# Kernel tuning notes

Hardware: AMD Instinct MI355X
Metric: run time of the kernel (lower is better)

Reference implementation:

```python
import jax, jax.numpy as jnp
import numpy as np
from jax import lax

IMG = 1024
STRIDES = (4, 8, 16, 32, 64)
SIZE_BASES = (32, 64, 128, 256, 512)
SCALES = (8.0,)
RATIOS = (0.5, 1.0, 2.0)
PRE_NMS = 2000
POST_NMS = 1000
NMS_THRESH = 0.7
B = 4


def _level_anchors(stride, size_base):
    """Anchors [G*G*A, 4] in xyxy, centered on grid cells."""
    g = IMG // stride
    cs = (jnp.arange(g, dtype=jnp.float32) + 0.5) * stride
    cy, cx = jnp.meshgrid(cs, cs, indexing='ij')          # [g,g]
    ctr = jnp.stack([cx.ravel(), cy.ravel()], axis=-1)    # [g*g, 2]
    wh = []
    for r in RATIOS:
        for s in SCALES:
            wh.append((size_base * s * np.sqrt(1.0 / r), size_base * s * np.sqrt(r)))
    wh = jnp.asarray(wh, jnp.float32)                     # [A, 2]
    x1y1 = ctr[:, None, :] - 0.5 * wh[None, :, :]
    x2y2 = ctr[:, None, :] + 0.5 * wh[None, :, :]
    return jnp.concatenate([x1y1, x2y2], axis=-1).reshape(-1, 4)


def _decode(anchors, deltas):
    wa = anchors[:, 2] - anchors[:, 0]
    ha = anchors[:, 3] - anchors[:, 1]
    cxa = anchors[:, 0] + 0.5 * wa
    cya = anchors[:, 1] + 0.5 * ha
    dx, dy, dw, dh = deltas[:, 0], deltas[:, 1], deltas[:, 2], deltas[:, 3]
    cx = dx * wa + cxa
    cy = dy * ha + cya
    w = jnp.exp(dw) * wa
    h = jnp.exp(dh) * ha
    return jnp.stack([cx - 0.5 * w, cy - 0.5 * h, cx + 0.5 * w, cy + 0.5 * h], axis=-1)


def _clip(boxes, info):
    h, w = info[0], info[1]
    x = jnp.clip(boxes[:, 0::2], 0.0, w - 1.0)
    y = jnp.clip(boxes[:, 1::2], 0.0, h - 1.0)
    return jnp.stack([x[:, 0], y[:, 0], x[:, 1], y[:, 1]], axis=-1)


def _iou_matrix(boxes):
    area = jnp.maximum(boxes[:, 2] - boxes[:, 0], 0.0) * jnp.maximum(boxes[:, 3] - boxes[:, 1], 0.0)
    lt = jnp.maximum(boxes[:, None, :2], boxes[None, :, :2])
    rb = jnp.minimum(boxes[:, None, 2:], boxes[None, :, 2:])
    wh = jnp.maximum(rb - lt, 0.0)
    inter = wh[..., 0] * wh[..., 1]
    return inter / jnp.maximum(area[:, None] + area[None, :] - inter, 1e-9)


def _nms_keep(boxes, thresh):
    """Boxes sorted by score desc. Returns boolean keep mask."""
    iou = _iou_matrix(boxes)
    n = boxes.shape[0]
    idx = jnp.arange(n)
    def body(i, keep):
        sup = keep[i] & (iou[i] > thresh) & (idx > i)
        return keep & ~sup
    return lax.fori_loop(0, n, body, jnp.ones((n,), bool))


def reference(probs0, probs1, probs2, probs3, probs4,
              reg0, reg1, reg2, reg3, reg4, img_info):
    anchors = [_level_anchors(s, b) for s, b in zip(STRIDES, SIZE_BASES)]
    probs = (probs0, probs1, probs2, probs3, probs4)
    regs = (reg0, reg1, reg2, reg3, reg4)

    def per_image(pr, rg, info):
        boxes_all, scores_all = [], []
        for a, p, r in zip(anchors, pr, rg):
            scores = p[:, 0]
            proposals = _clip(_decode(a, r), info)
            k = min(PRE_NMS, scores.shape[0])
            s, order = lax.top_k(scores, k)        # pre-NMS top-k, sorted desc
            bx = proposals[order]
            keep = _nms_keep(bx, NMS_THRESH)
            s = jnp.where(keep, s, -1.0)           # suppressed -> sentinel
            kp = min(POST_NMS, k)
            s2, o2 = lax.top_k(s, kp)              # post-NMS top-k per level
            boxes_all.append(bx[o2])
            scores_all.append(s2)
        ab = jnp.concatenate(boxes_all, axis=0)
        asc = jnp.concatenate(scores_all, axis=0)
        fs, fo = lax.top_k(asc, POST_NMS)          # merge levels, final top-k
        fb = jnp.where((fs >= 0.0)[:, None], ab[fo], 0.0)  # zero-pad invalid
        return fb

    fb = jax.vmap(per_image)(probs, regs, img_info)        # [B, POST, 4]
    bidx = jnp.broadcast_to(jnp.arange(B, dtype=fb.dtype)[:, None, None], (B, POST_NMS, 1))
    return jnp.concatenate([bidx, fb], axis=-1)            # [B, POST, 5]


def setup_inputs():
    key = jax.random.key(0)
    ks = jax.random.split(key, 10)
    grids = [IMG // s for s in STRIDES]
    A = [g * g * len(RATIOS) * len(SCALES) for g in grids]
    inp = {}
    for l in range(5):
        inp[f'probs{l}'] = jax.random.uniform(ks[l], (B, A[l], 2), dtype=jnp.float32)
        inp[f'reg{l}'] = 0.1 * jax.random.normal(ks[5 + l], (B, A[l], 4), dtype=jnp.float32)
    inp['img_info'] = jnp.tile(jnp.array([IMG, IMG, 1.0], jnp.float32), (B, 1))
    return inp
```

## Files before the change

### kernel.cpp

```cpp
#include <hip/hip_runtime.h>
#include <stdint.h>
#include <math.h>

#pragma clang fp contract(off)

#define NB 4
#define TOTA 261888
#define PRE 2000
#define POST 1000
#define CATN 4768
#define NBL 20
#define CANDCAP 4096
#define NBLK 4092
#define BPB 1023
#define HBLK 65

__device__ __forceinline__ unsigned keyF(float f) {
  unsigned u = __float_as_uint(f);
  return (u & 0x80000000u) ? ~u : (u | 0x80000000u);
}

__device__ __forceinline__ int lvlA(int l)   { switch (l) { case 0: return 196608; case 1: return 49152; case 2: return 12288; case 3: return 3072; default: return 768; } }
__device__ __forceinline__ int lvlOff(int l) { switch (l) { case 0: return 0; case 1: return 196608; case 2: return 245760; case 3: return 258048; default: return 261120; } }
__device__ __forceinline__ int lvlK(int l)   { return l == 4 ? 768 : 2000; }
__device__ __forceinline__ int lvlKP(int l)  { return l == 4 ? 768 : 1000; }
__device__ __forceinline__ int lvlBlkStart(int l) { switch (l) { case 0: return 0; case 1: return 768; case 2: return 960; case 3: return 1008; default: return 1020; } }
__device__ __forceinline__ int lvlBlkCnt(int l)   { switch (l) { case 0: return 768; case 1: return 192; case 2: return 48; case 3: return 12; default: return 3; } }

struct InPtrs {
  const float *p0, *p1, *p2, *p3, *p4;
  const float *r0, *r1, *r2, *r3, *r4;
  const float *info;
};

__device__ __forceinline__ void gaToLvl(int ga, int& l, int& off) {
  if (ga < 196608)      { l = 0; off = 0; }
  else if (ga < 245760) { l = 1; off = 196608; }
  else if (ga < 258048) { l = 2; off = 245760; }
  else if (ga < 261120) { l = 3; off = 258048; }
  else                  { l = 4; off = 261120; }
}

__device__ __forceinline__ void fatMap(int s, int& l, int& seg) {
  if (s < 48)      { l = 0; seg = s; }
  else if (s < 60) { l = 1; seg = s - 48; }
  else if (s < 63) { l = 2; seg = s - 60; }
  else if (s == 63){ l = 3; seg = 0; }
  else             { l = 4; seg = 0; }
}

__global__ __launch_bounds__(256) void k_decode(InPtrs P, float4* __restrict__ props,
                                                float* __restrict__ scores) {
  int gid = blockIdx.x * 256 + threadIdx.x;
  if (gid >= NB * TOTA) return;
  int b = gid / TOTA, ga = gid % TOTA;
  int Al, off, lg; float st; double S; const float *prp, *rgp;
  if (ga < 196608)      { Al = 196608; off = 0;      lg = 8; st = 4.0f;  S = 256.0;  prp = P.p0; rgp = P.r0; }
  else if (ga < 245760) { Al = 49152;  off = 196608; lg = 7; st = 8.0f;  S = 512.0;  prp = P.p1; rgp = P.r1; }
  else if (ga < 258048) { Al = 12288;  off = 245760; lg = 6; st = 16.0f; S = 1024.0; prp = P.p2; rgp = P.r2; }
  else if (ga < 261120) { Al = 3072;   off = 258048; lg = 5; st = 32.0f; S = 2048.0; prp = P.p3; rgp = P.r3; }
  else                  { Al = 768;    off = 261120; lg = 4; st = 64.0f; S = 4096.0; prp = P.p4; rgp = P.r4; }
  int i = ga - off;
  int cell = i / 3, rr = i - cell * 3;
  int col = cell & ((1 << lg) - 1), row = cell >> lg;
  float cx0 = ((float)col + 0.5f) * st;
  float cy0 = ((float)row + 0.5f) * st;
  const double SQ2 = 1.4142135623730951;
  const double SQH = 0.7071067811865476;
  double swd = (rr == 0) ? SQ2 : (rr == 1 ? 1.0 : SQH);
  double shd = (rr == 0) ? SQH : (rr == 1 ? 1.0 : SQ2);
  float wf = (float)(S * swd), hf = (float)(S * shd);
  float ax1 = cx0 - 0.5f * wf, ay1 = cy0 - 0.5f * hf;
  float ax2 = cx0 + 0.5f * wf, ay2 = cy0 + 0.5f * hf;
  size_t base = (size_t)b * Al + i;
  float sc = prp[base * 2];
  float4 d4 = ((const float4*)rgp)[base];
  float dx = d4.x, dy = d4.y, dw = d4.z, dh = d4.w;
  float wa = ax2 - ax1, ha = ay2 - ay1;
  float cxa = ax1 + 0.5f * wa, cya = ay1 + 0.5f * ha;
  float cx = dx * wa + cxa, cy = dy * ha + cya;
  float w = (float)exp((double)dw) * wa;
  float h = (float)exp((double)dh) * ha;
  float x1 = cx - 0.5f * w, y1 = cy - 0.5f * h;
  float x2 = cx + 0.5f * w, y2 = cy + 0.5f * h;
  float Hc = P.info[b * 3 + 0] - 1.0f, Wc = P.info[b * 3 + 1] - 1.0f;
  float4 o;
  o.x = fminf(fmaxf(x1, 0.0f), Wc);
  o.y = fminf(fmaxf(y1, 0.0f), Hc);
  o.z = fminf(fmaxf(x2, 0.0f), Wc);
  o.w = fminf(fmaxf(y2, 0.0f), Hc);
  props[gid] = o;
  scores[gid] = sc;
}

__global__ __launch_bounds__(256) void k_hist8(const float* __restrict__ scores,
                                               unsigned* __restrict__ hist8) {
  __shared__ unsigned h[256];
  int blk = blockIdx.x;
  int b = blk / HBLK, s = blk % HBLK;
  int l, seg; fatMap(s, l, seg);
  int n = lvlA(l), off = lvlOff(l);
  int start = seg * 4096;
  int cnt_s = min(4096, n - start);
  int tid = threadIdx.x;
  h[tid] = 0;
  __syncthreads();
  const float* sc = scores + (size_t)b * TOTA + off + start;
  for (int q = tid; q < cnt_s; q += 256)
    atomicAdd(&h[keyF(sc[q]) >> 24], 1u);
  __syncthreads();
  unsigned v = h[tid];
  if (v) atomicAdd(&hist8[(b * 5 + l) * 256 + tid], v);
}

__global__ __launch_bounds__(256) void k_thr8(const unsigned* __restrict__ hist8,
                                              unsigned* __restrict__ c1r1) {
  __shared__ unsigned h[256];
  int bl = blockIdx.x, tid = threadIdx.x;
  h[tid] = hist8[bl * 256 + tid];
  __syncthreads();
  if (tid == 0) {
    unsigned K = (unsigned)lvlK(bl % 5), cum = 0; int c;
    for (c = 255; c > 0; --c) { if (cum + h[c] >= K) break; cum += h[c]; }
    c1r1[bl * 2] = (unsigned)c;
    c1r1[bl * 2 + 1] = K - cum;
  }
}

__global__ __launch_bounds__(256) void k_hist6(const float* __restrict__ scores,
                                               const unsigned* __restrict__ c1r1,
                                               unsigned* __restrict__ hist6) {
  __shared__ unsigned h[64];
  int blk = blockIdx.x;
  int b = blk / HBLK, s = blk % HBLK;
  int l, seg; fatMap(s, l, seg);
  int n = lvlA(l), off = lvlOff(l);
  int start = seg * 4096;
  int cnt_s = min(4096, n - start);
  int tid = threadIdx.x;
  int bl = b * 5 + l;
  unsigned c1 = c1r1[bl * 2];
  if (tid < 64) h[tid] = 0;
  __syncthreads();
  const float* sc = scores + (size_t)b * TOTA + off + start;
  for (int q = tid; q < cnt_s; q += 256) {
    unsigned key = keyF(sc[q]);
    if ((key >> 24) == c1) atomicAdd(&h[(key >> 18) & 63u], 1u);
  }
  __syncthreads();
  if (tid < 64) {
    unsigned v = h[tid];
    if (v) atomicAdd(&hist6[bl * 64 + tid], v);
  }
}

__global__ __launch_bounds__(64) void k_thr6(const unsigned* __restrict__ hist6,
                                             const unsigned* __restrict__ c1r1,
                                             unsigned* __restrict__ T14) {
  __shared__ unsigned h[64];
  int bl = blockIdx.x, tid = threadIdx.x;
  h[tid] = hist6[bl * 64 + tid];
  __syncthreads();
  if (tid == 0) {
    unsigned r1 = c1r1[bl * 2 + 1], cum = 0; int c;
    for (c = 63; c > 0; --c) { if (cum + h[c] >= r1) break; cum += h[c]; }
    T14[bl] = (c1r1[bl * 2] << 6) | (unsigned)c;
  }
}

__global__ __launch_bounds__(256) void k_cnt(const float* __restrict__ scores,
                                             const unsigned* __restrict__ T14,
                                             unsigned* __restrict__ blockCnt) {
  __shared__ unsigned ws[4];
  int gid = blockIdx.x * 256 + threadIdx.x;
  int tid = threadIdx.x;
  int b = gid / TOTA, ga = gid % TOTA;
  int l, off; gaToLvl(ga, l, off);
  int bl = b * 5 + l;
  bool pred = (keyF(scores[gid]) >> 18) >= T14[bl];
  unsigned long long m = __ballot(pred);
  if ((tid & 63) == 0) ws[tid >> 6] = (unsigned)__popcll(m);
  __syncthreads();
  if (tid == 0) blockCnt[blockIdx.x] = ws[0] + ws[1] + ws[2] + ws[3];
}

__global__ __launch_bounds__(1024) void k_scanblk(const unsigned* __restrict__ blockCnt,
                                                  unsigned* __restrict__ blockBase,
                                                  unsigned* __restrict__ cnt) {
  __shared__ unsigned a[4096];
  __shared__ unsigned ch[1024];
  int tid = threadIdx.x;
  int q0 = tid * 4;
  unsigned a0 = (q0 + 0 < NBLK) ? blockCnt[q0 + 0] : 0u;
  unsigned a1 = (q0 + 1 < NBLK) ? blockCnt[q0 + 1] : 0u;
  unsigned a2 = (q0 + 2 < NBLK) ? blockCnt[q0 + 2] : 0u;
  unsigned a3 = (q0 + 3 < NBLK) ? blockCnt[q0 + 3] : 0u;
  unsigned p0 = a0, p1 = p0 + a1, p2 = p1 + a2, p3 = p2 + a3;
  ch[tid] = p3;
  __syncthreads();
  for (int d = 1; d < 1024; d <<= 1) {
    unsigned t = (tid >= d) ? ch[tid - d] : 0u;
    __syncthreads();
    ch[tid] += t;
    __syncthreads();
  }
  unsigned cbase = (tid > 0) ? ch[tid - 1] : 0u;
  a[q0 + 0] = cbase + p0;
  a[q0 + 1] = cbase + p1;
  a[q0 + 2] = cbase + p2;
  a[q0 + 3] = cbase + p3;
  __syncthreads();
  for (int k = 0; k < 4; ++k) {
    int g = q0 + k;
    if (g < NBLK) {
      int b = g / BPB, r = g % BPB;
      int l = (r < 768) ? 0 : (r < 960) ? 1 : (r < 1008) ? 2 : (r < 1020) ? 3 : 4;
      int ss = b * BPB + lvlBlkStart(l);
      unsigned Eg = (g > 0) ? a[g - 1] : 0u;
      unsigned Es = (ss > 0) ? a[ss - 1] : 0u;
      blockBase[g] = Eg - Es;
    }
  }
  if (tid < NBL) {
    int b = tid / 5, l = tid % 5;
    int ss = b * BPB + lvlBlkStart(l);
    int ee = ss + lvlBlkCnt(l);
    unsigned Ee = a[ee - 1];
    unsigned Es = (ss > 0) ? a[ss - 1] : 0u;
    cnt[tid] = Ee - Es;
  }
}

__global__ __launch_bounds__(256) void k_fill(const float* __restrict__ scores,
                                              const unsigned* __restrict__ T14,
                                              const unsigned* __restrict__ blockBase,
                                              unsigned long long* __restrict__ cand) {
  __shared__ unsigned ws[4];
  int gid = blockIdx.x * 256 + threadIdx.x;
  int tid = threadIdx.x;
  int b = gid / TOTA, ga = gid % TOTA;
  int l, off; gaToLvl(ga, l, off);
  int bl = b * 5 + l;
  unsigned key = keyF(scores[gid]);
  bool pred = (key >> 18) >= T14[bl];
  unsigned long long m = __ballot(pred);
  int wv = tid >> 6, ln = tid & 63;
  if (ln == 0) ws[wv] = (unsigned)__popcll(m);
  __syncthreads();
  unsigned wo = 0;
  for (int q = 0; q < wv; ++q) wo += ws[q];
  unsigned pre = (unsigned)__popcll(m & ((1ull << ln) - 1ull));
  if (pred) {
    unsigned p = blockBase[blockIdx.x] + wo + pre;
    if (p < CANDCAP)
      cand[(size_t)bl * CANDCAP + p] =
          ((unsigned long long)key << 32) | (unsigned long long)(0xFFFFFFFFu - (unsigned)(ga - off));
  }
}

__global__ __launch_bounds__(256) void k_sortc(unsigned long long* __restrict__ cand,
                                               const unsigned* __restrict__ cnt) {
  __shared__ unsigned long long arr[512];
  int blk = blockIdx.x;
  int bl = blk >> 3, ch = blk & 7;
  int base = ch * 512;
  int num = (int)min(cnt[bl], (unsigned)CANDCAP);
  int tid = threadIdx.x;
  unsigned long long* cp = cand + (size_t)bl * CANDCAP + base;
  for (int q = tid; q < 512; q += 256)
    arr[q] = (base + q < num) ? cp[q] : 0ull;
  __syncthreads();
  for (int kk = 2; kk <= 512; kk <<= 1)
    for (int jj = kk >> 1; jj > 0; jj >>= 1) {
      for (int idx = tid; idx < 512; idx += 256) {
        int p2 = idx ^ jj;
        if (p2 > idx) {
          unsigned long long x = arr[idx], y = arr[p2];
          bool up = (idx & kk) == 0;
          if (up ? (x < y) : (x > y)) { arr[idx] = y; arr[p2] = x; }
        }
      }
      __syncthreads();
    }
  for (int q = tid; q < 512; q += 256) cp[q] = arr[q];
}

__global__ __launch_bounds__(256) void k_rank(const unsigned long long* __restrict__ cand,
                                              const float4* __restrict__ props,
                                              const float* __restrict__ scores,
                                              float4* __restrict__ sBox,
                                              float* __restrict__ sArea,
                                              float* __restrict__ sScore) {
  int gid = blockIdx.x * 256 + threadIdx.x;
  int bl = gid >> 12, p = gid & 4095;
  int b = bl / 5, l = bl % 5;
  int K = lvlK(l), off = lvlOff(l);
  const unsigned long long* cp = cand + (size_t)bl * CANDCAP;
  unsigned long long me = cp[p];
  int ch = p >> 9;
  int rank = p & 511;
  for (int c2 = 0; c2 < 8; ++c2) {
    if (c2 == ch) continue;
    const unsigned long long* d = cp + c2 * 512;
    int lo = 0, hi = 512;
    while (lo < hi) {
      int mid = (lo + hi) >> 1;
      if (d[mid] > me) lo = mid + 1; else hi = mid;
    }
    rank += lo;
  }
  if (rank < K) {
    unsigned idx = 0xFFFFFFFFu - (unsigned)(me & 0xFFFFFFFFull);
    float4 bx = props[(size_t)b * TOTA + off + idx];
    float area = fmaxf(bx.z - bx.x, 0.0f) * fmaxf(bx.w - bx.y, 0.0f);
    sBox[bl * PRE + rank] = bx;
    sArea[bl * PRE + rank] = area;
    sScore[bl * PRE + rank] = scores[(size_t)b * TOTA + off + idx];
  }
}

__global__ __launch_bounds__(256) void k_mask(const float4* __restrict__ sBox,
                                              const float* __restrict__ sArea,
                                              unsigned long long* __restrict__ mask) {
  int bi = blockIdx.x;
  int bl = bi >> 8, rem = bi & 255, ic = rem >> 3, jc = rem & 7;
  int l = bl % 5, K = lvlK(l);
  int i0 = ic * 64, j0 = jc * 256;
  if (i0 >= K || j0 >= K) return;
  if (jc * 4 + 3 < ic) return;
  int tid = threadIdx.x;
  __shared__ float4 jb[256];
  __shared__ float ja[256];
  int jend = min(256, K - j0);
  if (tid < jend) { jb[tid] = sBox[bl * PRE + j0 + tid]; ja[tid] = sArea[bl * PRE + j0 + tid]; }
  int ln = tid & 63, wsub = tid >> 6;
  int i = i0 + ln;
  int jw = jc * 4 + wsub;
  bool iv = i < K;
  float4 bi4 = make_float4(0.0f, 0.0f, 0.0f, 0.0f);
  float ai = 0.0f;
  if (iv) { bi4 = sBox[bl * PRE + i]; ai = sArea[bl * PRE + i]; }
  __syncthreads();
  int jbase = wsub * 64;
  int lim = jend - jbase;
  if (lim > 64) lim = 64;
  unsigned long long wacc = 0ull;
#pragma unroll 4
  for (int t = 0; t < lim; ++t) {
    float4 b4 = jb[jbase + t];
    float aj = ja[jbase + t];
    int j = j0 + jbase + t;
    bool pred = false;
    if (j > i) {
      float ltx = fmaxf(bi4.x, b4.x), lty = fmaxf(bi4.y, b4.y);
      float rbx = fminf(bi4.z, b4.z), rby = fminf(bi4.w, b4.w);
      float wx = fmaxf(rbx - ltx, 0.0f), wy = fmaxf(rby - lty, 0.0f);
      float inter = wx * wy;
      float den = fmaxf(ai + aj - inter, 1e-9f);
      pred = (inter / den) > 0.7f;
    }
    wacc |= ((unsigned long long)(pred ? 1u : 0u)) << t;
  }
  if (iv && jw >= ic && lim > 0)
    mask[((size_t)bl * PRE + i) * 32 + jw] = wacc;
}

__global__ __launch_bounds__(1024) void k_nms(const unsigned long long* __restrict__ mask,
                                              const float4* __restrict__ sBox,
                                              const float* __restrict__ sScore,
                                              float* __restrict__ catScore,
                                              float4* __restrict__ catBox) {
  __shared__ unsigned long long diag[PRE];
  __shared__ unsigned long long remv[32];
  __shared__ int list[1000];
  __shared__ int sTotal;
  int bl = blockIdx.x, b = bl / 5, l = bl % 5;
  int K = lvlK(l), KP = lvlKP(l), co = l * 1000;
  int tid = threadIdx.x;
  const unsigned long long* mrow = mask + (size_t)bl * PRE * 32;
  int c = tid & 31, g = tid >> 5;
  int nw = (K + 63) >> 6;
  for (int r = tid; r < K; r += 1024) diag[r] = mrow[(size_t)r * 32 + (r >> 6)];
  if (tid < 32) remv[tid] = 0ull;
  __syncthreads();
  unsigned long long w0 = 0ull, w1 = 0ull, nw0 = 0ull, nw1 = 0ull;
  {
    bool act = (c > 0) && (c < nw);
    int row0 = g, row1 = g + 32;
    if (act && row0 < K) w0 = mrow[(size_t)row0 * 32 + c];
    if (act && row1 < K) w1 = mrow[(size_t)row1 * 32 + c];
  }
  for (int t = 0; t < nw; ++t) {
    nw0 = 0ull; nw1 = 0ull;
    if (t + 1 < nw) {
      bool actn = (c > t + 1) && (c < nw);
      int row0 = (t + 1) * 64 + g, row1 = row0 + 32;
      if (actn && row0 < K) nw0 = mrow[(size_t)row0 * 32 + c];
      if (actn && row1 < K) nw1 = mrow[(size_t)row1 * 32 + c];
    }
    if (tid < 64) {
      int dr = t * 64 + tid;
      unsigned long long d = (dr < K) ? diag[dr] : 0ull;
      unsigned long long local = remv[t];
      int lim = min(64, K - t * 64);
      unsigned long long validm = (lim >= 64) ? ~0ull : ((1ull << lim) - 1ull);
      unsigned long long todo = (~local) & validm;
      while (todo) {
        int i2 = __ffsll((long long)todo) - 1;
        unsigned lo2 = __builtin_amdgcn_readlane((unsigned)d, i2);
        unsigned hi2 = __builtin_amdgcn_readlane((unsigned)(d >> 32), i2);
        unsigned long long dd = ((unsigned long long)hi2 << 32) | (unsigned long long)lo2;
        local |= dd;
        todo &= ~dd;
        todo &= ~(1ull << i2);
      }
      if (tid == 0) remv[t] = local;
    }
    __syncthreads();
    {
      unsigned long long local = remv[t];
      bool act = (c > t) && (c < nw);
      if (act) {
        unsigned long long acc = 0ull;
        int row0 = t * 64 + g, row1 = row0 + 32;
        if (row0 < K && !((local >> g) & 1ull)) acc |= w0;
        if (row1 < K && !((local >> (g + 32)) & 1ull)) acc |= w1;
        if (acc) atomicOr(&remv[c], acc);
      }
    }
    __syncthreads();
    w0 = nw0; w1 = nw1;
  }
  if (tid < 64) {
    int lane = tid;
    bool lv = lane < 32;
    unsigned long long remw = lv ? remv[lane] : 0ull;
    unsigned long long valid = 0ull;
    if (lv) {
      int rem = K - lane * 64;
      valid = (rem >= 64) ? ~0ull : (rem <= 0 ? 0ull : ((1ull << rem) - 1ull));
    }
    unsigned long long keepw = (~remw) & valid;
    unsigned long long suppw = remw & valid;
    unsigned long long lmask = (1ull << lane) - 1ull;
    int base = 0;
    for (int w2 = 0; w2 < 32 && base < KP; ++w2) {
      unsigned long long word = __shfl(keepw, w2);
      int pre = __popcll(word & lmask);
      if (((word >> lane) & 1ull) && (base + pre) < KP) list[base + pre] = w2 * 64 + lane;
      base += __popcll(word);
    }
    int totalKept = base;
    if (totalKept < KP) {
      int b2 = totalKept;
      for (int w2 = 0; w2 < 32 && b2 < KP; ++w2) {
        unsigned long long word = __shfl(suppw, w2);
        int pre = __popcll(word & lmask);
        if (((word >> lane) & 1ull) && (b2 + pre) < KP) list[b2 + pre] = w2 * 64 + lane;
        b2 += __popcll(word);
      }
    }
    if (lane == 0) sTotal = totalKept;
  }
  __syncthreads();
  int totalKept = sTotal;
  for (int t = tid; t < KP; t += 1024) {
    int j = list[t];
    float s = (t < totalKept) ? sScore[bl * PRE + j] : -1.0f;
    catScore[b * CATN + co + t] = s;
    catBox[b * CATN + co + t] = sBox[bl * PRE + j];
  }
}

__global__ __launch_bounds__(256) void k_final(const float* __restrict__ catScore,
                                               const float4* __restrict__ catBox,
                                               float* __restrict__ out) {
  int gid = blockIdx.x * 256 + threadIdx.x;
  if (gid >= NB * CATN) return;
  int b = gid / CATN, p = gid % CATN;
  int c = p / 1000; if (c > 4) c = 4;
  const float* cs = catScore + (size_t)b * CATN;
  float s = cs[p];
  unsigned long long me = ((unsigned long long)keyF(s) << 32) |
                          (unsigned long long)(0xFFFFFFFFu - (unsigned)p);
  int rank = p - c * 1000;
  for (int c2 = 0; c2 < 5; ++c2) {
    if (c2 == c) continue;
    int base = c2 * 1000, len = (c2 == 4) ? 768 : 1000;
    int lo = 0, hi = len;
    while (lo < hi) {
      int mid = (lo + hi) >> 1;
      int q = base + mid;
      unsigned long long k2 = ((unsigned long long)keyF(cs[q]) << 32) |
                              (unsigned long long)(0xFFFFFFFFu - (unsigned)q);
      if (k2 > me) lo = mid + 1; else hi = mid;
    }
    rank += lo;
  }
  if (rank < POST) {
    float4 bx = make_float4(0.0f, 0.0f, 0.0f, 0.0f);
    if (s >= 0.0f) bx = catBox[(size_t)b * CATN + p];
    float* o = out + ((size_t)b * POST + rank) * 5;
    o[0] = (float)b; o[1] = bx.x; o[2] = bx.y; o[3] = bx.z; o[4] = bx.w;
  }
}

extern "C" void kernel_launch(void* const* d_in, const int* in_sizes, int n_in,
                              void* d_out, int out_size, void* d_ws, size_t ws_size,
                              hipStream_t stream) {
  const int prSz[5] = {1572864, 393216, 98304, 24576, 6144};
  const int rgSz[5] = {3145728, 786432, 196608, 49152, 12288};
  const float* pr[5] = {nullptr, nullptr, nullptr, nullptr, nullptr};
  const float* rg[5] = {nullptr, nullptr, nullptr, nullptr, nullptr};
  const float* info = nullptr;
  for (int i = 0; i < n_in; ++i) {
    int s = in_sizes[i];
    bool m = false;
    for (int l = 0; l < 5; ++l) {
      if (s == prSz[l]) { pr[l] = (const float*)d_in[i]; m = true; break; }
      if (s == rgSz[l]) { rg[l] = (const float*)d_in[i]; m = true; break; }
    }
    if (!m && s == 12) info = (const float*)d_in[i];
  }
  InPtrs P;
  P.p0 = pr[0]; P.p1 = pr[1]; P.p2 = pr[2]; P.p3 = pr[3]; P.p4 = pr[4];
  P.r0 = rg[0]; P.r1 = rg[1]; P.r2 = rg[2]; P.r3 = rg[3]; P.r4 = rg[4];
  P.info = info;

  char* w = (char*)d_ws;
  float4* props = (float4*)w;                         w += (size_t)NB * TOTA * 16;
  float4* sBox = (float4*)w;                          w += (size_t)NBL * PRE * 16;
  float4* catBox = (float4*)w;                        w += (size_t)NB * CATN * 16;
  unsigned long long* mask = (unsigned long long*)w;  w += (size_t)NBL * PRE * 32 * 8;
  unsigned long long* cand = (unsigned long long*)w;  w += (size_t)NBL * CANDCAP * 8;
  float* scores = (float*)w;                          w += (size_t)NB * TOTA * 4;
  float* sArea = (float*)w;                           w += (size_t)NBL * PRE * 4;
  float* sScore = (float*)w;                          w += (size_t)NBL * PRE * 4;
  float* catScore = (float*)w;                        w += (size_t)NB * CATN * 4;
  unsigned* hist8 = (unsigned*)w;                     w += (size_t)NBL * 256 * 4;
  unsigned* hist6 = (unsigned*)w;                     w += (size_t)NBL * 64 * 4;
  unsigned* c1r1 = (unsigned*)w;                      w += (size_t)NBL * 2 * 4;
  unsigned* T14 = (unsigned*)w;                       w += (size_t)NBL * 4;
  unsigned* blockCnt = (unsigned*)w;                  w += (size_t)NBLK * 4;
  unsigned* blockBase = (unsigned*)w;                 w += (size_t)NBLK * 4;
  unsigned* cnt = (unsigned*)w;                       w += (size_t)NBL * 4;
  (void)ws_size; (void)out_size;

  hipMemsetAsync(hist8, 0, (size_t)NBL * (256 + 64) * 4, stream);

  k_decode<<<(NB * TOTA + 255) / 256, 256, 0, stream>>>(P, props, scores);
  k_hist8<<<NB * HBLK, 256, 0, stream>>>(scores, hist8);
  k_thr8<<<NBL, 256, 0, stream>>>(hist8, c1r1);
  k_hist6<<<NB * HBLK, 256, 0, stream>>>(scores, c1r1, hist6);
  k_thr6<<<NBL, 64, 0, stream>>>(hist6, c1r1, T14);
  k_cnt<<<NBLK, 256, 0, stream>>>(scores, T14, blockCnt);
  k_scanblk<<<1, 1024, 0, stream>>>(blockCnt, blockBase, cnt);
  k_fill<<<NBLK, 256, 0, stream>>>(scores, T14, blockBase, cand);
  k_sortc<<<NBL * 8, 256, 0, stream>>>(cand, cnt);
  k_rank<<<NBL * CANDCAP / 256, 256, 0, stream>>>(cand, props, scores, sBox, sArea, sScore);
  k_mask<<<NBL * 256, 256, 0, stream>>>(sBox, sArea, mask);
  k_nms<<<NBL, 1024, 0, stream>>>(mask, sBox, sScore, catScore, catBox);
  k_final<<<(NB * CATN + 255) / 256, 256, 0, stream>>>(catScore, catBox, (float*)d_out);
}
```

Baseline: 197.9 us.

## Drop precomputed IoU mask; compute suppression on the fly inside NMS kernel

Removes the separate k_mask kernel and the global IoU bitmask. The NMS kernel now loads boxes and areas into shared memory and computes only the per-tile diagonal masks. For each 64-box tile it then resolves the kept boxes serially, and every thread tests its own two candidate boxes against each kept box. This removes one launch and the large mask writes and reads, and it only computes IoU for boxes that are actually kept. In exchange, the IoU work now runs serially inside 20 blocks instead of being spread across many blocks.

Result: slower. 451.3 us (+128.0%).

```diff
diff --git a/kernel.cpp b/kernel.cpp
--- a/kernel.cpp
+++ b/kernel.cpp
@@ -319,92 +319,81 @@
   }
 }
 
-__global__ __launch_bounds__(256) void k_mask(const float4* __restrict__ sBox,
-                                              const float* __restrict__ sArea,
-                                              unsigned long long* __restrict__ mask) {
-  int bi = blockIdx.x;
-  int bl = bi >> 8, rem = bi & 255, ic = rem >> 3, jc = rem & 7;
-  int l = bl % 5, K = lvlK(l);
-  int i0 = ic * 64, j0 = jc * 256;
-  if (i0 >= K || j0 >= K) return;
-  if (jc * 4 + 3 < ic) return;
-  int tid = threadIdx.x;
-  __shared__ float4 jb[256];
-  __shared__ float ja[256];
-  int jend = min(256, K - j0);
-  if (tid < jend) { jb[tid] = sBox[bl * PRE + j0 + tid]; ja[tid] = sArea[bl * PRE + j0 + tid]; }
-  int ln = tid & 63, wsub = tid >> 6;
-  int i = i0 + ln;
-  int jw = jc * 4 + wsub;
-  bool iv = i < K;
-  float4 bi4 = make_float4(0.0f, 0.0f, 0.0f, 0.0f);
-  float ai = 0.0f;
-  if (iv) { bi4 = sBox[bl * PRE + i]; ai = sArea[bl * PRE + i]; }
-  __syncthreads();
-  int jbase = wsub * 64;
-  int lim = jend - jbase;
-  if (lim > 64) lim = 64;
-  unsigned long long wacc = 0ull;
-#pragma unroll 4
-  for (int t = 0; t < lim; ++t) {
-    float4 b4 = jb[jbase + t];
-    float aj = ja[jbase + t];
-    int j = j0 + jbase + t;
-    bool pred = false;
-    if (j > i) {
-      float ltx = fmaxf(bi4.x, b4.x), lty = fmaxf(bi4.y, b4.y);
-      float rbx = fminf(bi4.z, b4.z), rby = fminf(bi4.w, b4.w);
-      float wx = fmaxf(rbx - ltx, 0.0f), wy = fmaxf(rby - lty, 0.0f);
-      float inter = wx * wy;
-      float den = fmaxf(ai + aj - inter, 1e-9f);
-      pred = (inter / den) > 0.7f;
-    }
-    wacc |= ((unsigned long long)(pred ? 1u : 0u)) << t;
-  }
-  if (iv && jw >= ic && lim > 0)
-    mask[((size_t)bl * PRE + i) * 32 + jw] = wacc;
-}
-
-__global__ __launch_bounds__(1024) void k_nms(const unsigned long long* __restrict__ mask,
-                                              const float4* __restrict__ sBox,
+__global__ __launch_bounds__(1024) void k_nms(const float4* __restrict__ sBoxG,
+                                              const float* __restrict__ sAreaG,
                                               const float* __restrict__ sScore,
                                               float* __restrict__ catScore,
                                               float4* __restrict__ catBox) {
+  __shared__ float4 bx[PRE];
+  __shared__ float  ar[PRE];
   __shared__ unsigned long long diag[PRE];
-  __shared__ unsigned long long remv[32];
+  __shared__ unsigned long long keepw[32];
   __shared__ int list[1000];
   __shared__ int sTotal;
   int bl = blockIdx.x, b = bl / 5, l = bl % 5;
   int K = lvlK(l), KP = lvlKP(l), co = l * 1000;
   int tid = threadIdx.x;
-  const unsigned long long* mrow = mask + (size_t)bl * PRE * 32;
-  int c = tid & 31, g = tid >> 5;
+  int wave = tid >> 6, ln = tid & 63;
   int nw = (K + 63) >> 6;
-  for (int r = tid; r < K; r += 1024) diag[r] = mrow[(size_t)r * 32 + (r >> 6)];
-  if (tid < 32) remv[tid] = 0ull;
-  __syncthreads();
-  unsigned long long w0 = 0ull, w1 = 0ull, nw0 = 0ull, nw1 = 0ull;
-  {
-    bool act = (c > 0) && (c < nw);
-    int row0 = g, row1 = g + 32;
-    if (act && row0 < K) w0 = mrow[(size_t)row0 * 32 + c];
-    if (act && row1 < K) w1 = mrow[(size_t)row1 * 32 + c];
-  }
+  for (int r = tid; r < K; r += 1024) { bx[r] = sBoxG[bl * PRE + r]; ar[r] = sAreaG[bl * PRE + r]; }
+  if (tid < 32) keepw[tid] = 0ull;
+  __syncthreads();
+  for (int p = 0; p < 2; ++p) {
+    int tt = p * 16 + wave;
+    if (tt < nw) {
+      int base = tt * 64;
+      int r = base + ln;
+      bool iv = r < K;
+      float4 bi4 = make_float4(0.0f, 0.0f, 0.0f, 0.0f);
+      float ai = 0.0f;
+      if (iv) { bi4 = bx[r]; ai = ar[r]; }
+      int lim = min(64, K - base);
+      unsigned long long wacc = 0ull;
+      for (int t = 0; t < lim; ++t) {
+        float4 b4 = bx[base + t];
+        float aj = ar[base + t];
+        bool pred = false;
+        if (iv && t > ln) {
+          float ltx = fmaxf(bi4.x, b4.x), lty = fmaxf(bi4.y, b4.y);
+          float rbx = fminf(bi4.z, b4.z), rby = fminf(bi4.w, b4.w);
+          float wx = fmaxf(rbx - ltx, 0.0f), wy = fmaxf(rby - lty, 0.0f);
+          float inter = wx * wy;
+          float den = fmaxf(ai + aj - inter, 1e-9f);
+          pred = (inter / den) > 0.7f;
+        }
+        wacc |= ((unsigned long long)(pred ? 1u : 0u)) << t;
+      }
+      if (iv) diag[r] = wacc;
+    }
+  }
+  int j1 = tid, j2 = 1024 + tid;
+  bool v1 = j1 < K, v2 = j2 < K;
+  float4 bj1 = make_float4(0.0f, 0.0f, 0.0f, 0.0f), bj2 = bj1;
+  float aj1 = 0.0f, aj2 = 0.0f;
+  if (v1) { bj1 = bx[j1]; aj1 = ar[j1]; }
+  if (v2) { bj2 = bx[j2]; aj2 = ar[j2]; }
+  bool rm1 = false, rm2 = false;
+  __syncthreads();
   for (int t = 0; t < nw; ++t) {
-    nw0 = 0ull; nw1 = 0ull;
-    if (t + 1 < nw) {
-      bool actn = (c > t + 1) && (c < nw);
-      int row0 = (t + 1) * 64 + g, row1 = row0 + 32;
-      if (actn && row0 < K) nw0 = mrow[(size_t)row0 * 32 + c];
-      if (actn && row1 < K) nw1 = mrow[(size_t)row1 * 32 + c];
-    }
+    if (t < 16) {
+      if (wave == t) {
+        unsigned long long m = __ballot(rm1);
+        if (ln == 0) keepw[t] = m;
+      }
+    } else {
+      if (wave == t - 16) {
+        unsigned long long m = __ballot(rm2);
+        if (ln == 0) keepw[t] = m;
+      }
+    }
+    __syncthreads();
     if (tid < 64) {
       int dr = t * 64 + tid;
       unsigned long long d = (dr < K) ? diag[dr] : 0ull;
-      unsigned long long local = remv[t];
+      unsigned long long local = keepw[t];
       int lim = min(64, K - t * 64);
-      unsigned long long validm = (lim >= 64) ? ~0ull : ((1ull << lim) - 1ull);
-      unsigned long long todo = (~local) & validm;
+      unsigned long long vm = (lim >= 64) ? ~0ull : ((1ull << lim) - 1ull);
+      unsigned long long todo = (~local) & vm;
       while (todo) {
         int i2 = __ffsll((long long)todo) - 1;
         unsigned lo2 = __builtin_amdgcn_readlane((unsigned)d, i2);
@@ -414,38 +403,50 @@
         todo &= ~dd;
         todo &= ~(1ull << i2);
       }
-      if (tid == 0) remv[t] = local;
+      if (tid == 0) keepw[t] = (~local) & vm;
     }
     __syncthreads();
-    {
-      unsigned long long local = remv[t];
-      bool act = (c > t) && (c < nw);
-      if (act) {
-        unsigned long long acc = 0ull;
-        int row0 = t * 64 + g, row1 = row0 + 32;
-        if (row0 < K && !((local >> g) & 1ull)) acc |= w0;
-        if (row1 < K && !((local >> (g + 32)) & 1ull)) acc |= w1;
-        if (acc) atomicOr(&remv[c], acc);
-      }
-    }
-    __syncthreads();
-    w0 = nw0; w1 = nw1;
-  }
+    unsigned long long kw = keepw[t];
+    while (kw) {
+      int i2 = __ffsll((long long)kw) - 1;
+      kw &= kw - 1;
+      int i = t * 64 + i2;
+      float4 b4 = bx[i];
+      float ai = ar[i];
+      if (v1 && j1 > i && !rm1) {
+        float ltx = fmaxf(b4.x, bj1.x), lty = fmaxf(b4.y, bj1.y);
+        float rbx = fminf(b4.z, bj1.z), rby = fminf(b4.w, bj1.w);
+        float wx = fmaxf(rbx - ltx, 0.0f), wy = fmaxf(rby - lty, 0.0f);
+        float inter = wx * wy;
+        float den = fmaxf(ai + aj1 - inter, 1e-9f);
+        rm1 = (inter / den) > 0.7f;
+      }
+      if (v2 && j2 > i && !rm2) {
+        float ltx = fmaxf(b4.x, bj2.x), lty = fmaxf(b4.y, bj2.y);
+        float rbx = fminf(b4.z, bj2.z), rby = fminf(b4.w, bj2.w);
+        float wx = fmaxf(rbx - ltx, 0.0f), wy = fmaxf(rby - lty, 0.0f);
+        float inter = wx * wy;
+        float den = fmaxf(ai + aj2 - inter, 1e-9f);
+        rm2 = (inter / den) > 0.7f;
+      }
+    }
+  }
+  __syncthreads();
   if (tid < 64) {
     int lane = tid;
     bool lv = lane < 32;
-    unsigned long long remw = lv ? remv[lane] : 0ull;
+    unsigned long long kwv = lv ? keepw[lane] : 0ull;
     unsigned long long valid = 0ull;
     if (lv) {
       int rem = K - lane * 64;
       valid = (rem >= 64) ? ~0ull : (rem <= 0 ? 0ull : ((1ull << rem) - 1ull));
     }
-    unsigned long long keepw = (~remw) & valid;
-    unsigned long long suppw = remw & valid;
+    unsigned long long keep2 = kwv;
+    unsigned long long supp2 = (~kwv) & valid;
     unsigned long long lmask = (1ull << lane) - 1ull;
     int base = 0;
     for (int w2 = 0; w2 < 32 && base < KP; ++w2) {
-      unsigned long long word = __shfl(keepw, w2);
+      unsigned long long word = __shfl(keep2, w2);
       int pre = __popcll(word & lmask);
       if (((word >> lane) & 1ull) && (base + pre) < KP) list[base + pre] = w2 * 64 + lane;
       base += __popcll(word);
@@ -454,7 +455,7 @@
     if (totalKept < KP) {
       int b2 = totalKept;
       for (int w2 = 0; w2 < 32 && b2 < KP; ++w2) {
-        unsigned long long word = __shfl(suppw, w2);
+        unsigned long long word = __shfl(supp2, w2);
         int pre = __popcll(word & lmask);
         if (((word >> lane) & 1ull) && (b2 + pre) < KP) list[b2 + pre] = w2 * 64 + lane;
         b2 += __popcll(word);
@@ -468,7 +469,7 @@
     int j = list[t];
     float s = (t < totalKept) ? sScore[bl * PRE + j] : -1.0f;
     catScore[b * CATN + co + t] = s;
-    catBox[b * CATN + co + t] = sBox[bl * PRE + j];
+    catBox[b * CATN + co + t] = bx[j];
   }
 }
 
@@ -531,7 +532,6 @@
   float4* props = (float4*)w;                         w += (size_t)NB * TOTA * 16;
   float4* sBox = (float4*)w;                          w += (size_t)NBL * PRE * 16;
   float4* catBox = (float4*)w;                        w += (size_t)NB * CATN * 16;
-  unsigned long long* mask = (unsigned long long*)w;  w += (size_t)NBL * PRE * 32 * 8;
   unsigned long long* cand = (unsigned long long*)w;  w += (size_t)NBL * CANDCAP * 8;
   float* scores = (float*)w;                          w += (size_t)NB * TOTA * 4;
   float* sArea = (float*)w;                           w += (size_t)NBL * PRE * 4;
@@ -558,7 +558,6 @@
   k_fill<<<NBLK, 256, 0, stream>>>(scores, T14, blockBase, cand);
   k_sortc<<<NBL * 8, 256, 0, stream>>>(cand, cnt);
   k_rank<<<NBL * CANDCAP / 256, 256, 0, stream>>>(cand, props, scores, sBox, sArea, sScore);
-  k_mask<<<NBL * 256, 256, 0, stream>>>(sBox, sArea, mask);
-  k_nms<<<NBL, 1024, 0, stream>>>(mask, sBox, sScore, catScore, catBox);
+  k_nms<<<NBL, 1024, 0, stream>>>(sBox, sArea, sScore, catScore, catBox);
   k_final<<<(NB * CATN + 255) / 256, 256, 0, stream>>>(catScore, catBox, (float*)d_out);
 }
```
